# Optimization experiments

Hardware: AMD Instinct MI355X
Metric: run time of the kernel (lower is better)

## Reference

```python
import jax, jax.numpy as jnp
import numpy as np


def _lovasz_softmax_flat(probas, labels):
    # probas: [P, C] softmax probabilities; labels: [P] int class ids
    P, C = probas.shape
    classes = jnp.arange(C)
    # fg[c, p] = 1 if pixel p has ground-truth class c
    fg = (labels[None, :] == classes[:, None]).astype(probas.dtype)      # [C, P]
    errors = jnp.abs(fg - probas.T)                                       # [C, P]
    # sort errors descending per class, permute fg the same way
    order = jnp.argsort(-errors, axis=1)                                  # [C, P]
    errors_sorted = jnp.take_along_axis(errors, order, axis=1)
    fg_sorted = jnp.take_along_axis(fg, order, axis=1)
    # Lovasz gradient of the Jaccard loss w.r.t. sorted errors
    gts = jnp.sum(fg_sorted, axis=1, keepdims=True)                       # [C, 1]
    intersection = gts - jnp.cumsum(fg_sorted, axis=1)
    union = gts + jnp.cumsum(1.0 - fg_sorted, axis=1)
    jaccard = 1.0 - intersection / union                                  # [C, P]
    jaccard = jnp.concatenate([jaccard[:, :1], jaccard[:, 1:] - jaccard[:, :-1]], axis=1)
    # grad is treated as constant w.r.t. probas (matches torch Variable(grad) detach)
    jaccard = jax.lax.stop_gradient(jaccard)
    losses = jnp.sum(errors_sorted * jaccard, axis=1)                     # [C]
    # classes='present': average only over classes present in the labels
    present = (gts[:, 0] > 0).astype(probas.dtype)
    return jnp.sum(losses * present) / jnp.maximum(jnp.sum(present), 1.0)


def reference(input, target):
    B, C, H, W = input.shape
    probas = jax.nn.softmax(input, axis=1)                                # [B, C, H, W]
    probas_flat = probas.transpose(0, 2, 3, 1).reshape(-1, C)             # [P, C]
    labels_flat = target.reshape(-1)                                      # [P]
    return _lovasz_softmax_flat(probas_flat, labels_flat)


def setup_inputs() -> dict:
    key = jax.random.key(0)
    k1, k2 = jax.random.split(key)
    B, C, H, W = 8, 19, 512, 512
    inp = jax.random.normal(k1, (B, C, H, W), dtype=jnp.float32)
    tgt = jax.random.randint(k2, (B, H, W), 0, C, dtype=jnp.int64)
    return {"input": inp, "target": tgt}
```

## Files before the change

### kernel.cpp

```cpp
#include <hip/hip_runtime.h>
#include <stdint.h>


#define C_CLASSES 19
#define NBINS 768
#define HISTWORDS (C_CLASSES * NBINS)
#define HW_SHIFT 18
#define HW_MASK ((1 << HW_SHIFT) - 1)
#define NGROUPS 8

__global__ __launch_bounds__(1024) void k1_hist(
    const float* __restrict__ x, const int* __restrict__ labels,
    unsigned int* __restrict__ copies, int P, int pixPerBlk)
{
    __shared__ unsigned int hist[HISTWORDS];
    int tid = threadIdx.x;
    for (int i = tid; i < HISTWORDS; i += 1024) hist[i] = 0u;
    __syncthreads();

    int base = blockIdx.x * pixPerBlk;
    for (int it = 0; it < pixPerBlk; it += 1024) {
        int p = base + it + tid;
        if (p < P) {
            int lab = labels[p];
            int img = p >> HW_SHIFT;
            int rem = p & HW_MASK;
            const float* xp = x + (((size_t)img * C_CLASSES) << HW_SHIFT) + rem;
            float r[C_CLASSES];
            float m = -1e30f;
#pragma unroll
            for (int c = 0; c < C_CLASSES; ++c) {
                r[c] = xp[(size_t)c << HW_SHIFT];
                m = fmaxf(m, r[c]);
            }
            float s = 0.f;
#pragma unroll
            for (int c = 0; c < C_CLASSES; ++c) { r[c] = __expf(r[c] - m); s += r[c]; }
            float inv = 1.f / s;
#pragma unroll
            for (int c = 0; c < C_CLASSES; ++c) {
                float pr = r[c] * inv;
                bool fg = (c == lab);
                float err = fg ? (1.f - pr) : pr;
                int idx = __float2int_rn(err * (float)(NBINS - 1));
                idx = idx < 0 ? 0 : (idx > NBINS - 1 ? NBINS - 1 : idx);
                atomicAdd(&hist[c * NBINS + idx], fg ? 0x10001u : 1u);
            }
        }
    }
    __syncthreads();
    unsigned int* dst = copies + (size_t)blockIdx.x * HISTWORDS;
    for (int i = tid; i < HISTWORDS; i += 1024) dst[i] = hist[i];
}

__global__ __launch_bounds__(256) void k2_reduce(
    const unsigned int* __restrict__ copies,
    int* __restrict__ nPart, int* __restrict__ fPart,
    int ncopies, int cpg)
{
    int pos = blockIdx.x * 256 + threadIdx.x;
    int g = blockIdx.y;
    int c0 = g * cpg;
    int c1 = c0 + cpg; if (c1 > ncopies) c1 = ncopies;
    unsigned int sn = 0, sf = 0;
    for (int k = c0; k < c1; ++k) {
        unsigned int w = copies[(size_t)k * HISTWORDS + pos];
        sn += w & 0xFFFFu;
        sf += w >> 16;
    }
    nPart[(size_t)g * HISTWORDS + pos] = (int)sn;
    fPart[(size_t)g * HISTWORDS + pos] = (int)sf;
}

__global__ __launch_bounds__(64) void k3_scan(
    const int* __restrict__ nPart, const int* __restrict__ fPart,
    float* __restrict__ res)
{
    int c = blockIdx.x;
    int lane = threadIdx.x;
    const int PER = NBINS / 64;
    int nl[PER], fl[PER];
    int totN = 0, totF = 0;
#pragma unroll
    for (int i = 0; i < PER; ++i) {
        int j = lane * PER + i;
        int bin = NBINS - 1 - j;
        int pos = c * NBINS + bin;
        int n = 0, f = 0;
#pragma unroll
        for (int g = 0; g < NGROUPS; ++g) {
            n += nPart[g * HISTWORDS + pos];
            f += fPart[g * HISTWORDS + pos];
        }
        nl[i] = n; fl[i] = f; totN += n; totF += f;
    }
    int incN = totN, incF = totF;
    for (int off = 1; off < 64; off <<= 1) {
        int tn = __shfl_up(incN, off);
        int tf = __shfl_up(incF, off);
        if (lane >= off) { incN += tn; incF += tf; }
    }
    int G = __shfl(incF, 63);
    double loss = 0.0;
    if (G > 0) {
        int cumN = incN - totN;
        int cumF = incF - totF;
        double dG = (double)G;
        double Jb = 1.0 - (dG - (double)cumF) / (dG + (double)cumN - (double)cumF);
#pragma unroll
        for (int i = 0; i < PER; ++i) {
            int bin = NBINS - 1 - (lane * PER + i);
            cumN += nl[i]; cumF += fl[i];
            double Ja = 1.0 - (dG - (double)cumF) / (dG + (double)cumN - (double)cumF);
            loss += ((double)bin / (double)(NBINS - 1)) * (Ja - Jb);
            Jb = Ja;
        }
    }
    for (int off = 32; off > 0; off >>= 1)
        loss += __shfl_down(loss, off);
    if (lane == 0) { res[c] = (float)loss; res[C_CLASSES + c] = (float)G; }
}

__global__ void k4_final(const float* __restrict__ res, float* __restrict__ out)
{
    if (threadIdx.x == 0 && blockIdx.x == 0) {
        float s = 0.f, cnt = 0.f;
        for (int c = 0; c < C_CLASSES; ++c) {
            if (res[C_CLASSES + c] > 0.f) { s += res[c]; cnt += 1.f; }
        }
        out[0] = s / fmaxf(cnt, 1.f);
    }
}

extern "C" void kernel_launch(void* const* d_in, const int* in_sizes, int n_in,
                              void* d_out, int out_size, void* d_ws, size_t ws_size,
                              hipStream_t stream)
{
    const float* x = (const float*)d_in[0];
    const int* labels = (const int*)d_in[1];
    float* out = (float*)d_out;
    int P = in_sizes[1];

    const size_t histBytes = (size_t)HISTWORDS * 4;
    const size_t partBytes = (size_t)NGROUPS * HISTWORDS * 4;
    const size_t resBytes = 2 * C_CLASSES * 4;
    const size_t reserved = 2 * partBytes + resBytes + 256;

    int maxCopies = (int)((ws_size > reserved ? ws_size - reserved : 0) / histBytes);
    int ncopies = maxCopies < 512 ? maxCopies : 512;
    if (ncopies < 1) ncopies = 1;
    int pixPerBlk = (P + ncopies - 1) / ncopies;
    pixPerBlk = ((pixPerBlk + 1023) / 1024) * 1024;

    unsigned int* copies = (unsigned int*)d_ws;
    int* nPart = (int*)((char*)d_ws + histBytes * (size_t)ncopies);
    int* fPart = (int*)((char*)nPart + partBytes);
    float* res = (float*)((char*)fPart + partBytes);

    int cpg = (ncopies + NGROUPS - 1) / NGROUPS;

    k1_hist<<<dim3(ncopies), dim3(1024), 0, stream>>>(x, labels, copies, P, pixPerBlk);
    k2_reduce<<<dim3(HISTWORDS / 256, NGROUPS), dim3(256), 0, stream>>>(copies, nPart, fPart, ncopies, cpg);
    k3_scan<<<dim3(C_CLASSES), dim3(64), 0, stream>>>(nPart, fPart, res);
    k4_final<<<dim3(1), dim3(64), 0, stream>>>(res, out);
}
```

Before: 253.5 us.

## Vectorize histogram loads to four pixels per thread and fuse final reduction into scan

Each thread in the histogram kernel now loads four adjacent pixels with float4/int4 loads and processes them through a shared helper. The helper uses a fast reciprocal and computes the foreground bin by mirroring the index instead of subtracting from one. Block count drops from 512 to 256 to match the larger per-thread work, and the shared-memory zeroing and copy-out use uint4. The separate final kernel is removed: the last scan block, chosen by an atomic ticket that the reduce kernel resets, computes the output, saving one launch. The costs are higher register pressure from four live 19-float arrays, fewer blocks to hide latency, and slight rounding differences in bin indices.

```diff
diff --git a/kernel.cpp b/kernel.cpp
--- a/kernel.cpp
+++ b/kernel.cpp
@@ -9,55 +9,89 @@
 #define HW_MASK ((1 << HW_SHIFT) - 1)
 #define NGROUPS 8
 
+__device__ __forceinline__ void px_process(float* r, float m, int lab,
+                                           unsigned int* hist)
+{
+    float s = 0.f;
+#pragma unroll
+    for (int c = 0; c < C_CLASSES; ++c) {
+        float t = __expf(r[c] - m);
+        r[c] = t;
+        s += t;
+    }
+    float scale = (float)(NBINS - 1) * __builtin_amdgcn_rcpf(s);
+#pragma unroll
+    for (int c = 0; c < C_CLASSES; ++c) {
+        int ti = __float2int_rn(r[c] * scale);
+        int idx = (c == lab) ? (NBINS - 1 - ti) : ti;
+        idx = idx < 0 ? 0 : (idx > NBINS - 1 ? NBINS - 1 : idx);
+        atomicAdd(&hist[c * NBINS + idx], (c == lab) ? 0x10001u : 1u);
+    }
+}
+
 __global__ __launch_bounds__(1024) void k1_hist(
     const float* __restrict__ x, const int* __restrict__ labels,
     unsigned int* __restrict__ copies, int P, int pixPerBlk)
 {
     __shared__ unsigned int hist[HISTWORDS];
     int tid = threadIdx.x;
-    for (int i = tid; i < HISTWORDS; i += 1024) hist[i] = 0u;
+    uint4* h4 = (uint4*)hist;
+    for (int i = tid; i < HISTWORDS / 4; i += 1024) h4[i] = make_uint4(0u, 0u, 0u, 0u);
     __syncthreads();
 
     int base = blockIdx.x * pixPerBlk;
-    for (int it = 0; it < pixPerBlk; it += 1024) {
-        int p = base + it + tid;
-        if (p < P) {
-            int lab = labels[p];
-            int img = p >> HW_SHIFT;
-            int rem = p & HW_MASK;
+    for (int it = 0; it < pixPerBlk; it += 4096) {
+        int pix = base + it + tid * 4;
+        if (pix + 3 < P) {
+            int img = pix >> HW_SHIFT;
+            int rem = pix & HW_MASK;
             const float* xp = x + (((size_t)img * C_CLASSES) << HW_SHIFT) + rem;
-            float r[C_CLASSES];
-            float m = -1e30f;
+            float r0[C_CLASSES], r1[C_CLASSES], r2[C_CLASSES], r3[C_CLASSES];
+            float m0 = -3.4e38f, m1 = -3.4e38f, m2 = -3.4e38f, m3 = -3.4e38f;
 #pragma unroll
             for (int c = 0; c < C_CLASSES; ++c) {
-                r[c] = xp[(size_t)c << HW_SHIFT];
-                m = fmaxf(m, r[c]);
+                float4 v = *reinterpret_cast<const float4*>(xp + ((size_t)c << HW_SHIFT));
+                r0[c] = v.x; r1[c] = v.y; r2[c] = v.z; r3[c] = v.w;
+                m0 = fmaxf(m0, v.x); m1 = fmaxf(m1, v.y);
+                m2 = fmaxf(m2, v.z); m3 = fmaxf(m3, v.w);
             }
-            float s = 0.f;
-#pragma unroll
-            for (int c = 0; c < C_CLASSES; ++c) { r[c] = __expf(r[c] - m); s += r[c]; }
-            float inv = 1.f / s;
-#pragma unroll
-            for (int c = 0; c < C_CLASSES; ++c) {
-                float pr = r[c] * inv;
-                bool fg = (c == lab);
-                float err = fg ? (1.f - pr) : pr;
-                int idx = __float2int_rn(err * (float)(NBINS - 1));
-                idx = idx < 0 ? 0 : (idx > NBINS - 1 ? NBINS - 1 : idx);
-                atomicAdd(&hist[c * NBINS + idx], fg ? 0x10001u : 1u);
+            int4 lb = *reinterpret_cast<const int4*>(labels + pix);
+            px_process(r0, m0, lb.x, hist);
+            px_process(r1, m1, lb.y, hist);
+            px_process(r2, m2, lb.z, hist);
+            px_process(r3, m3, lb.w, hist);
+        } else {
+#pragma unroll
+            for (int k = 0; k < 4; ++k) {
+                int p = pix + k;
+                if (p < P) {
+                    int img = p >> HW_SHIFT;
+                    int rem = p & HW_MASK;
+                    const float* xp = x + (((size_t)img * C_CLASSES) << HW_SHIFT) + rem;
+                    float r[C_CLASSES];
+                    float m = -3.4e38f;
+#pragma unroll
+                    for (int c = 0; c < C_CLASSES; ++c) {
+                        r[c] = xp[(size_t)c << HW_SHIFT];
+                        m = fmaxf(m, r[c]);
+                    }
+                    px_process(r, m, labels[p], hist);
+                }
             }
         }
     }
     __syncthreads();
-    unsigned int* dst = copies + (size_t)blockIdx.x * HISTWORDS;
-    for (int i = tid; i < HISTWORDS; i += 1024) dst[i] = hist[i];
+    uint4* dst = (uint4*)(copies + (size_t)blockIdx.x * HISTWORDS);
+    const uint4* src = (const uint4*)hist;
+    for (int i = tid; i < HISTWORDS / 4; i += 1024) dst[i] = src[i];
 }
 
 __global__ __launch_bounds__(256) void k2_reduce(
     const unsigned int* __restrict__ copies,
     int* __restrict__ nPart, int* __restrict__ fPart,
-    int ncopies, int cpg)
-{
+    int* __restrict__ ticket, int ncopies, int cpg)
+{
+    if (blockIdx.x == 0 && blockIdx.y == 0 && threadIdx.x == 0) *ticket = 0;
     int pos = blockIdx.x * 256 + threadIdx.x;
     int g = blockIdx.y;
     int c0 = g * cpg;
@@ -74,7 +108,8 @@
 
 __global__ __launch_bounds__(64) void k3_scan(
     const int* __restrict__ nPart, const int* __restrict__ fPart,
-    float* __restrict__ res)
+    float* __restrict__ res, int* __restrict__ ticket,
+    float* __restrict__ out)
 {
     int c = blockIdx.x;
     int lane = threadIdx.x;
@@ -118,17 +153,21 @@
     }
     for (int off = 32; off > 0; off >>= 1)
         loss += __shfl_down(loss, off);
-    if (lane == 0) { res[c] = (float)loss; res[C_CLASSES + c] = (float)G; }
-}
-
-__global__ void k4_final(const float* __restrict__ res, float* __restrict__ out)
-{
-    if (threadIdx.x == 0 && blockIdx.x == 0) {
-        float s = 0.f, cnt = 0.f;
-        for (int c = 0; c < C_CLASSES; ++c) {
-            if (res[C_CLASSES + c] > 0.f) { s += res[c]; cnt += 1.f; }
-        }
-        out[0] = s / fmaxf(cnt, 1.f);
+    if (lane == 0) {
+        __hip_atomic_store(&res[c], (float)loss, __ATOMIC_RELAXED, __HIP_MEMORY_SCOPE_AGENT);
+        __hip_atomic_store(&res[C_CLASSES + c], (float)G, __ATOMIC_RELAXED, __HIP_MEMORY_SCOPE_AGENT);
+        int t = __hip_atomic_fetch_add(ticket, 1, __ATOMIC_ACQ_REL, __HIP_MEMORY_SCOPE_AGENT);
+        if (t == C_CLASSES - 1) {
+            float s = 0.f, cnt = 0.f;
+            for (int cc = 0; cc < C_CLASSES; ++cc) {
+                float g = __hip_atomic_load(&res[C_CLASSES + cc], __ATOMIC_RELAXED, __HIP_MEMORY_SCOPE_AGENT);
+                if (g > 0.f) {
+                    s += __hip_atomic_load(&res[cc], __ATOMIC_RELAXED, __HIP_MEMORY_SCOPE_AGENT);
+                    cnt += 1.f;
+                }
+            }
+            out[0] = s / fmaxf(cnt, 1.f);
+        }
     }
 }
 
@@ -143,24 +182,24 @@
 
     const size_t histBytes = (size_t)HISTWORDS * 4;
     const size_t partBytes = (size_t)NGROUPS * HISTWORDS * 4;
-    const size_t resBytes = 2 * C_CLASSES * 4;
+    const size_t resBytes = 256;
     const size_t reserved = 2 * partBytes + resBytes + 256;
 
     int maxCopies = (int)((ws_size > reserved ? ws_size - reserved : 0) / histBytes);
-    int ncopies = maxCopies < 512 ? maxCopies : 512;
+    int ncopies = maxCopies < 256 ? maxCopies : 256;
     if (ncopies < 1) ncopies = 1;
     int pixPerBlk = (P + ncopies - 1) / ncopies;
-    pixPerBlk = ((pixPerBlk + 1023) / 1024) * 1024;
+    pixPerBlk = ((pixPerBlk + 4095) / 4096) * 4096;
 
     unsigned int* copies = (unsigned int*)d_ws;
     int* nPart = (int*)((char*)d_ws + histBytes * (size_t)ncopies);
     int* fPart = (int*)((char*)nPart + partBytes);
     float* res = (float*)((char*)fPart + partBytes);
+    int* ticket = (int*)((char*)res + 160);
 
     int cpg = (ncopies + NGROUPS - 1) / NGROUPS;
 
     k1_hist<<<dim3(ncopies), dim3(1024), 0, stream>>>(x, labels, copies, P, pixPerBlk);
-    k2_reduce<<<dim3(HISTWORDS / 256, NGROUPS), dim3(256), 0, stream>>>(copies, nPart, fPart, ncopies, cpg);
-    k3_scan<<<dim3(C_CLASSES), dim3(64), 0, stream>>>(nPart, fPart, res);
-    k4_final<<<dim3(1), dim3(64), 0, stream>>>(res, out);
-}
+    k2_reduce<<<dim3(HISTWORDS / 256, NGROUPS), dim3(256), 0, stream>>>(copies, nPart, fPart, ticket, ncopies, cpg);
+    k3_scan<<<dim3(C_CLASSES), dim3(64), 0, stream>>>(nPart, fPart, res, ticket, out);
+}
```

Result: faster. 247.7 us (-2.3%).
